# Kernel optimization log

Measured on AMD Instinct MI355X. Metric: run time of the kernel, lower is better.

Reference implementation:

```python
import jax, jax.numpy as jnp
import numpy as np

NV, NE = 4096, 8192
IN_V, OUT_V, IN_E = 128, 128, 64

def setup_inputs() -> dict:
    key = jax.random.key(0)
    ks = jax.random.split(key, 8)
    stdv = 1.0 / np.sqrt(OUT_V)
    return {
        "H_v": jax.random.normal(ks[0], (NV, IN_V), dtype=jnp.float32),
        "H_e": jax.random.normal(ks[1], (NE, IN_E), dtype=jnp.float32),
        "adj_e": jax.random.uniform(ks[2], (NE, NE), dtype=jnp.float32),
        "adj_v": jax.random.uniform(ks[3], (NV, NV), dtype=jnp.float32),
        "T": jax.random.uniform(ks[4], (NV, NE), dtype=jnp.float32),
        "weight": jax.random.uniform(ks[5], (IN_V, OUT_V), minval=-stdv, maxval=stdv, dtype=jnp.float32),
        "bias": jax.random.uniform(ks[6], (OUT_V,), minval=-stdv, maxval=stdv, dtype=jnp.float32),
        "p": jax.random.normal(ks[7], (1, IN_E), dtype=jnp.float32),
    }

def reference(H_v, H_e, adj_e, adj_v, T, weight, bias, p):
    # node_layer=True path of GraphConvolution.forward
    # diag_values = (H_e @ p.T).T[0]  -> [Ne]
    d = H_e @ p[0]                                   # [Ne]
    # T @ diag(d) @ T^T  ==  (T * d) @ T^T  (avoid materializing NxN diag)
    multiplier1 = (T * d[None, :]) @ T.T             # [Nv, Nv]
    # M1 = eye*1 + (1-eye)*multiplier1  -> set diagonal to 1
    idx = jnp.arange(multiplier1.shape[0])
    M1 = multiplier1.at[idx, idx].set(1.0)
    adjusted_A = M1 * adj_v                          # [Nv, Nv]
    output = adjusted_A @ (H_v @ weight) + bias      # [Nv, out_v]
    return (output, H_e)
```

## Files before the change

kernel.cpp:

```cpp
#include <hip/hip_runtime.h>
#include <cstdint>
#include <cstddef>

#define NV 4096
#define NE 8192
#define INV 128
#define OUTV 128
#define INE 64

#define BK 64
#define NT (NE / BK)
#define HALF_B 16384
#define LDS_BYTES (9 * HALF_B)

typedef __bf16 bf16x8 __attribute__((ext_vector_type(8)));
typedef float f32x4 __attribute__((ext_vector_type(4)));

__device__ __forceinline__ uint16_t f2bf(float x) {
  uint32_t u = __builtin_bit_cast(uint32_t, x);
  u += 0x7fff + ((u >> 16) & 1);
  return (uint16_t)(u >> 16);
}

__global__ void k_diag(const float* __restrict__ He, const float* __restrict__ p,
                       float* __restrict__ d) {
  int lane = threadIdx.x & 63;
  int wid = threadIdx.x >> 6;
  int row = blockIdx.x * 4 + wid;
  float v = He[(size_t)row * INE + lane] * p[lane];
#pragma unroll
  for (int off = 32; off; off >>= 1) v += __shfl_xor(v, off);
  if (lane == 0) d[row] = v;
}

__global__ void k_prep(const float4* __restrict__ T4, const float4* __restrict__ d4,
                       ushort4* __restrict__ A4, ushort4* __restrict__ B4) {
  const size_t total = (size_t)NV * NE / 4;
  size_t stride = (size_t)gridDim.x * blockDim.x;
  for (size_t i = (size_t)blockIdx.x * blockDim.x + threadIdx.x; i < total; i += stride) {
    float4 t = T4[i];
    float4 dv = d4[i & (NE / 4 - 1)];
    ushort4 a, b;
    b.x = f2bf(t.x); b.y = f2bf(t.y); b.z = f2bf(t.z); b.w = f2bf(t.w);
    a.x = f2bf(t.x * dv.x); a.y = f2bf(t.y * dv.y);
    a.z = f2bf(t.z * dv.z); a.w = f2bf(t.w * dv.w);
    A4[i] = a;
    B4[i] = b;
  }
}

__global__ void k_xw(const float* __restrict__ Hv, const float* __restrict__ W,
                     uint16_t* __restrict__ XT) {
  __shared__ float row[INV];
  int m = blockIdx.x;
  int n = threadIdx.x;
  row[n] = Hv[(size_t)m * INV + n];
  __syncthreads();
  float acc = 0.f;
#pragma unroll 8
  for (int k = 0; k < INV; ++k) acc += row[k] * W[k * OUTV + n];
  XT[(size_t)n * NV + m] = f2bf(acc);
}


__device__ __forceinline__ void gload16(const char* src, char* ldst) {
  __builtin_amdgcn_global_load_lds(
      (const __attribute__((address_space(1))) uint32_t*)src,
      (__attribute__((address_space(3))) uint32_t*)ldst, 16, 0, 0);
}

__global__ __launch_bounds__(512, 2) void k_gemm1(const uint16_t* __restrict__ A,
                                                  const uint16_t* __restrict__ B,
                                                  const float* __restrict__ adj_v,
                                                  uint16_t* __restrict__ adjA) {
  extern __shared__ char smem[];
  char* Aslot = smem;
  char* Bslot = smem + 5 * HALF_B;

  const int tid = threadIdx.x;
  const int lane = tid & 63, wid = tid >> 6;
  const int wr = wid >> 2, wc = wid & 3;
  const int lr = lane & 15, lk = lane >> 4;
  const int bcol0 = (wc & 1) * 64;

  int bid = blockIdx.x;
  int xcd = bid & 7, cid = bid >> 3;
  int bi = (xcd >> 1) * 4 + (cid >> 3);
  int bj = (xcd & 1) * 8 + (cid & 7);

  const int arow0 = bi * 256, brow0 = bj * 256;

  const int swz0 = ((lk) ^ (lr & 7)) << 4;
  const int swz1 = ((4 + lk) ^ (lr & 7)) << 4;
  const int pA0 = lr * 128 + swz0;
  const int pA1 = lr * 128 + swz1;
  const int pB0 = (bcol0 + lr) * 128 + swz0;
  const int pB1 = (bcol0 + lr) * 128 + swz1;

  const int srow = tid >> 3;
  const int sslot = (tid & 7) ^ (srow & 7);
  const int soff0 = srow * 16384 + sslot * 16;
  const int soff1 = soff0 + 64 * 16384;
  const char* Abase = (const char*)A + (size_t)arow0 * 16384;
  const char* Bbase = (const char*)B + (size_t)brow0 * 16384;
  const int ld0 = tid * 16;
  const int ld1 = tid * 16 + 8192;

  f32x4 acc[8][4] = {};
  bf16x8 af[4][2], af2[4][2], bfr[2][2], bfr2[2][2];

  {
    gload16(Abase + soff0, Aslot + ld0);
    gload16(Abase + soff1, Aslot + ld1);
    gload16(Abase + 2097152 + soff0, Aslot + HALF_B + ld0);
    gload16(Abase + 2097152 + soff1, Aslot + HALF_B + ld1);
    gload16(Bbase + soff0, Bslot + ld0);
    gload16(Bbase + soff1, Bslot + ld1);
    gload16(Bbase + 2097152 + soff0, Bslot + HALF_B + ld0);
    gload16(Bbase + 2097152 + soff1, Bslot + HALF_B + ld1);
    gload16(Abase + 128 + soff0, Aslot + 2 * HALF_B + ld0);
    gload16(Abase + 128 + soff1, Aslot + 2 * HALF_B + ld1);
  }
  asm volatile("s_waitcnt vmcnt(2)" ::: "memory");
  asm volatile("s_barrier" ::: "memory");

  int sA = 0;
  int sB = 0;
  for (int t = 0; t < NT; ++t) {
    const char* aB = Aslot + (((sA + wr) >= 5) ? (sA + wr - 5) : (sA + wr)) * HALF_B;
    const char* bB = Bslot + ((sB + (wc >> 1)) & 3) * HALF_B;
    const char* aK0 = aB + pA0;
    const char* aK1 = aB + pA1;
    const char* bK0 = bB + pB0;
    const char* bK1 = bB + pB1;
    const int k1 = (t + 1) * 128;
    const int k2 = (t + 2) * 128;

#pragma unroll
    for (int m = 0; m < 4; ++m) {
      af[m][0] = *(const bf16x8*)(aK0 + m * 2048);
      af[m][1] = *(const bf16x8*)(aK1 + m * 2048);
    }
#pragma unroll
    for (int n = 0; n < 2; ++n) {
      bfr[n][0] = *(const bf16x8*)(bK0 + n * 2048);
      bfr[n][1] = *(const bf16x8*)(bK1 + n * 2048);
    }
    if (t + 1 < NT) {
      int s1 = sA + 3; if (s1 >= 5) s1 -= 5;
      char* dA1 = Aslot + s1 * HALF_B;
      gload16(Abase + 2097152 + k1 + soff0, dA1 + ld0);
      gload16(Abase + 2097152 + k1 + soff1, dA1 + ld1);
      char* dB0 = Bslot + ((sB + 2) & 3) * HALF_B;
      gload16(Bbase + k1 + soff0, dB0 + ld0);
      gload16(Bbase + k1 + soff1, dB0 + ld1);
      char* dB1 = Bslot + ((sB + 3) & 3) * HALF_B;
      gload16(Bbase + 2097152 + k1 + soff0, dB1 + ld0);
      gload16(Bbase + 2097152 + k1 + soff1, dB1 + ld1);
    }
    __builtin_amdgcn_s_setprio(1);
#pragma unroll
    for (int m = 0; m < 4; ++m)
#pragma unroll
      for (int n = 0; n < 2; ++n)
#pragma unroll
        for (int kk = 0; kk < 2; ++kk)
          acc[m][n] = __builtin_amdgcn_mfma_f32_16x16x32_bf16(af[m][kk], bfr[n][kk], acc[m][n], 0, 0, 0);
    __builtin_amdgcn_s_setprio(0);

#pragma unroll
    for (int n = 0; n < 2; ++n) {
      bfr2[n][0] = *(const bf16x8*)(bK0 + 4096 + n * 2048);
      bfr2[n][1] = *(const bf16x8*)(bK1 + 4096 + n * 2048);
    }
    if (t + 2 < NT) {
      int s2 = sA + 4; if (s2 >= 5) s2 -= 5;
      char* dA0 = Aslot + s2 * HALF_B;
      gload16(Abase + k2 + soff0, dA0 + ld0);
      gload16(Abase + k2 + soff1, dA0 + ld1);
    }
    __builtin_amdgcn_s_setprio(1);
#pragma unroll
    for (int m = 0; m < 4; ++m)
#pragma unroll
      for (int n = 0; n < 2; ++n)
#pragma unroll
        for (int kk = 0; kk < 2; ++kk)
          acc[m][2 + n] = __builtin_amdgcn_mfma_f32_16x16x32_bf16(af[m][kk], bfr2[n][kk], acc[m][2 + n], 0, 0, 0);
    __builtin_amdgcn_s_setprio(0);

#pragma unroll
    for (int m = 0; m < 4; ++m) {
      af2[m][0] = *(const bf16x8*)(aK0 + 8192 + m * 2048);
      af2[m][1] = *(const bf16x8*)(aK1 + 8192 + m * 2048);
    }
    __builtin_amdgcn_s_setprio(1);
#pragma unroll
    for (int m = 0; m < 4; ++m)
#pragma unroll
      for (int n = 0; n < 2; ++n)
#pragma unroll
        for (int kk = 0; kk < 2; ++kk)
          acc[4 + m][2 + n] = __builtin_amdgcn_mfma_f32_16x16x32_bf16(af2[m][kk], bfr2[n][kk], acc[4 + m][2 + n], 0, 0, 0);
    __builtin_amdgcn_s_setprio(0);

    __builtin_amdgcn_s_setprio(1);
#pragma unroll
    for (int m = 0; m < 4; ++m)
#pragma unroll
      for (int n = 0; n < 2; ++n)
#pragma unroll
        for (int kk = 0; kk < 2; ++kk)
          acc[4 + m][n] = __builtin_amdgcn_mfma_f32_16x16x32_bf16(af2[m][kk], bfr[n][kk], acc[4 + m][n], 0, 0, 0);
    __builtin_amdgcn_s_setprio(0);

    if (t + 2 < NT) {
      asm volatile("s_waitcnt vmcnt(2)" ::: "memory");
    } else {
      asm volatile("s_waitcnt vmcnt(0)" ::: "memory");
    }
    asm volatile("s_barrier" ::: "memory");

    sA += 2; if (sA >= 5) sA -= 5;
    sB ^= 2;
  }

#pragma unroll
  for (int m = 0; m < 8; ++m) {
    int grow0 = bi * 256 + wr * 128 + m * 16 + lk * 4;
#pragma unroll
    for (int n = 0; n < 4; ++n) {
      int gcol = bj * 256 + wc * 64 + n * 16 + lr;
#pragma unroll
      for (int r = 0; r < 4; ++r) {
        int grow = grow0 + r;
        float v = acc[m][n][r];
        if (grow == gcol) v = 1.0f;
        adjA[(size_t)grow * NV + gcol] = f2bf(v * adj_v[(size_t)grow * NV + gcol]);
      }
    }
  }
}

__global__ __launch_bounds__(256) void k_gemm2p(const uint16_t* __restrict__ A,
                                                const uint16_t* __restrict__ B,
                                                float* __restrict__ part) {
  __shared__ __align__(16) uint16_t As[128 * 32];
  __shared__ __align__(16) uint16_t Bs[128 * 32];
  const int tid = threadIdx.x;
  const int wid = tid >> 6, lane = tid & 63;
  const int wr = wid >> 1, wc = wid & 1;
  const int ks = blockIdx.x & 7;
  const int bi = blockIdx.x >> 3;
  const int lr = lane & 15, lk = lane >> 4;

  f32x4 acc[4][4] = {};

  for (int kt = ks * 16; kt < ks * 16 + 16; ++kt) {
#pragma unroll
    for (int i = 0; i < 2; ++i) {
      int o = (wid * 2 + i) * 1024 + lane * 16;
      int row = o >> 6, kb = o & 63;
      const char* ga = (const char*)A + ((size_t)(bi * 128 + row) * NV + kt * 32) * 2 + kb;
      const char* gb = (const char*)B + ((size_t)row * NV + kt * 32) * 2 + kb;
      __builtin_amdgcn_global_load_lds(
          (const __attribute__((address_space(1))) uint32_t*)ga,
          (__attribute__((address_space(3))) uint32_t*)((char*)As + (wid * 2 + i) * 1024),
          16, 0, 0);
      __builtin_amdgcn_global_load_lds(
          (const __attribute__((address_space(1))) uint32_t*)gb,
          (__attribute__((address_space(3))) uint32_t*)((char*)Bs + (wid * 2 + i) * 1024),
          16, 0, 0);
    }
    __syncthreads();
    bf16x8 af[4], bfr[4];
#pragma unroll
    for (int m = 0; m < 4; ++m)
      af[m] = *(const bf16x8*)&As[(wr * 64 + m * 16 + lr) * 32 + lk * 8];
#pragma unroll
    for (int n = 0; n < 4; ++n)
      bfr[n] = *(const bf16x8*)&Bs[(wc * 64 + n * 16 + lr) * 32 + lk * 8];
#pragma unroll
    for (int m = 0; m < 4; ++m)
#pragma unroll
      for (int n = 0; n < 4; ++n)
        acc[m][n] = __builtin_amdgcn_mfma_f32_16x16x32_bf16(af[m], bfr[n], acc[m][n], 0, 0, 0);
    __syncthreads();
  }

  float* my = part + (size_t)ks * NV * OUTV;
#pragma unroll
  for (int m = 0; m < 4; ++m) {
    int grow0 = bi * 128 + wr * 64 + m * 16 + lk * 4;
#pragma unroll
    for (int n = 0; n < 4; ++n) {
      int gcol = wc * 64 + n * 16 + lr;
#pragma unroll
      for (int r = 0; r < 4; ++r)
        my[(size_t)(grow0 + r) * OUTV + gcol] = acc[m][n][r];
    }
  }
}

__global__ void k_gemm2r(const float4* __restrict__ part, const float* __restrict__ bias,
                         float4* __restrict__ out) {
  int i = blockIdx.x * 256 + threadIdx.x;
  float4 s = part[i];
#pragma unroll
  for (int ks = 1; ks < 8; ++ks) {
    float4 q = part[(size_t)ks * (NV * OUTV / 4) + i];
    s.x += q.x; s.y += q.y; s.z += q.z; s.w += q.w;
  }
  float4 b = ((const float4*)bias)[i & 31];
  s.x += b.x; s.y += b.y; s.z += b.z; s.w += b.w;
  out[i] = s;
}

extern "C" void kernel_launch(void* const* d_in, const int* in_sizes, int n_in,
                              void* d_out, int out_size, void* d_ws, size_t ws_size,
                              hipStream_t stream) {
  const float* Hv = (const float*)d_in[0];
  const float* He = (const float*)d_in[1];
  const float* adj_v = (const float*)d_in[3];
  const float* T = (const float*)d_in[4];
  const float* W = (const float*)d_in[5];
  const float* bias = (const float*)d_in[6];
  const float* p = (const float*)d_in[7];
  float* out = (float*)d_out;

  char* ws = (char*)d_ws;
  float* dvec = (float*)ws;
  uint16_t* XT = (uint16_t*)(ws + 32768);
  uint16_t* Abf = (uint16_t*)(ws + 32768 + (1u << 20));
  uint16_t* Bbf = Abf + (size_t)NV * NE;
  uint16_t* adjA = Bbf + (size_t)NV * NE;
  float* part = (float*)Abf;

  static int lds_attr_set = 0;
  if (!lds_attr_set) {
    hipFuncSetAttribute((const void*)k_gemm1,
                        hipFuncAttributeMaxDynamicSharedMemorySize, LDS_BYTES);
    lds_attr_set = 1;
  }

  k_diag<<<NE / 4, 256, 0, stream>>>(He, p, dvec);
  k_prep<<<2048, 256, 0, stream>>>((const float4*)T, (const float4*)dvec,
                                   (ushort4*)Abf, (ushort4*)Bbf);
  k_xw<<<NV, INV, 0, stream>>>(Hv, W, XT);
  k_gemm1<<<256, 512, LDS_BYTES, stream>>>(Abf, Bbf, adj_v, adjA);
  k_gemm2p<<<256, 256, 0, stream>>>(adjA, XT, part);
  k_gemm2r<<<NV * OUTV / 4 / 256, 256, 0, stream>>>((const float4*)part, bias, (float4*)out);
  hipMemcpyAsync(out + (size_t)NV * OUTV, He, (size_t)NE * INE * sizeof(float),
                 hipMemcpyDeviceToDevice, stream);
}
```

Before: 297.1 us.

## Load B fragments directly from global memory instead of staging through LDS

The B operand of the main GEMM is no longer copied into LDS slots. Each wave now loads its B MFMA fragments straight from global memory into registers every K step, and LDS drops from nine half-buffers to five. This removes LDS traffic and capacity for B and may allow more occupancy, but B reads are now per-wave global loads that are not shared across waves, and their latency is exposed without prefetching. The MFMA and A-fragment load order is also rearranged.

```diff
diff --git a/kernel.cpp b/kernel.cpp
--- a/kernel.cpp
+++ b/kernel.cpp
@@ -11,7 +11,7 @@
 #define BK 64
 #define NT (NE / BK)
 #define HALF_B 16384
-#define LDS_BYTES (9 * HALF_B)
+#define LDS_BYTES (5 * HALF_B)
 
 typedef __bf16 bf16x8 __attribute__((ext_vector_type(8)));
 typedef float f32x4 __attribute__((ext_vector_type(4)));
@@ -75,7 +75,6 @@
                                                   uint16_t* __restrict__ adjA) {
   extern __shared__ char smem[];
   char* Aslot = smem;
-  char* Bslot = smem + 5 * HALF_B;
 
   const int tid = threadIdx.x;
   const int lane = tid & 63, wid = tid >> 6;
@@ -94,84 +93,61 @@
   const int swz1 = ((4 + lk) ^ (lr & 7)) << 4;
   const int pA0 = lr * 128 + swz0;
   const int pA1 = lr * 128 + swz1;
-  const int pB0 = (bcol0 + lr) * 128 + swz0;
-  const int pB1 = (bcol0 + lr) * 128 + swz1;
 
   const int srow = tid >> 3;
   const int sslot = (tid & 7) ^ (srow & 7);
   const int soff0 = srow * 16384 + sslot * 16;
   const int soff1 = soff0 + 64 * 16384;
   const char* Abase = (const char*)A + (size_t)arow0 * 16384;
-  const char* Bbase = (const char*)B + (size_t)brow0 * 16384;
   const int ld0 = tid * 16;
   const int ld1 = tid * 16 + 8192;
 
+  const uint16_t* Bpan = B + (size_t)brow0 * NE;
+  int bvoff[4];
+#pragma unroll
+  for (int n = 0; n < 4; ++n)
+    bvoff[n] = ((wc >> 1) * 128 + bcol0 + n * 16 + lr) * NE + lk * 8;
+
   f32x4 acc[8][4] = {};
   bf16x8 af[4][2], af2[4][2], bfr[2][2], bfr2[2][2];
 
-  {
-    gload16(Abase + soff0, Aslot + ld0);
-    gload16(Abase + soff1, Aslot + ld1);
-    gload16(Abase + 2097152 + soff0, Aslot + HALF_B + ld0);
-    gload16(Abase + 2097152 + soff1, Aslot + HALF_B + ld1);
-    gload16(Bbase + soff0, Bslot + ld0);
-    gload16(Bbase + soff1, Bslot + ld1);
-    gload16(Bbase + 2097152 + soff0, Bslot + HALF_B + ld0);
-    gload16(Bbase + 2097152 + soff1, Bslot + HALF_B + ld1);
-    gload16(Abase + 128 + soff0, Aslot + 2 * HALF_B + ld0);
-    gload16(Abase + 128 + soff1, Aslot + 2 * HALF_B + ld1);
-  }
+  gload16(Abase + soff0, Aslot + ld0);
+  gload16(Abase + soff1, Aslot + ld1);
+  gload16(Abase + 2097152 + soff0, Aslot + HALF_B + ld0);
+  gload16(Abase + 2097152 + soff1, Aslot + HALF_B + ld1);
+  gload16(Abase + 128 + soff0, Aslot + 2 * HALF_B + ld0);
+  gload16(Abase + 128 + soff1, Aslot + 2 * HALF_B + ld1);
   asm volatile("s_waitcnt vmcnt(2)" ::: "memory");
   asm volatile("s_barrier" ::: "memory");
 
   int sA = 0;
-  int sB = 0;
   for (int t = 0; t < NT; ++t) {
     const char* aB = Aslot + (((sA + wr) >= 5) ? (sA + wr - 5) : (sA + wr)) * HALF_B;
-    const char* bB = Bslot + ((sB + (wc >> 1)) & 3) * HALF_B;
     const char* aK0 = aB + pA0;
     const char* aK1 = aB + pA1;
-    const char* bK0 = bB + pB0;
-    const char* bK1 = bB + pB1;
+    const uint16_t* Bt = Bpan + t * 64;
     const int k1 = (t + 1) * 128;
     const int k2 = (t + 2) * 128;
+
+#pragma unroll
+    for (int n = 0; n < 2; ++n) {
+      bfr[n][0] = *(const bf16x8*)(Bt + bvoff[n]);
+      bfr[n][1] = *(const bf16x8*)(Bt + bvoff[n] + 32);
+      bfr2[n][0] = *(const bf16x8*)(Bt + bvoff[2 + n]);
+      bfr2[n][1] = *(const bf16x8*)(Bt + bvoff[2 + n] + 32);
+    }
 
 #pragma unroll
     for (int m = 0; m < 4; ++m) {
       af[m][0] = *(const bf16x8*)(aK0 + m * 2048);
       af[m][1] = *(const bf16x8*)(aK1 + m * 2048);
     }
-#pragma unroll
-    for (int n = 0; n < 2; ++n) {
-      bfr[n][0] = *(const bf16x8*)(bK0 + n * 2048);
-      bfr[n][1] = *(const bf16x8*)(bK1 + n * 2048);
-    }
+
     if (t + 1 < NT) {
       int s1 = sA + 3; if (s1 >= 5) s1 -= 5;
       char* dA1 = Aslot + s1 * HALF_B;
       gload16(Abase + 2097152 + k1 + soff0, dA1 + ld0);
       gload16(Abase + 2097152 + k1 + soff1, dA1 + ld1);
-      char* dB0 = Bslot + ((sB + 2) & 3) * HALF_B;
-      gload16(Bbase + k1 + soff0, dB0 + ld0);
-      gload16(Bbase + k1 + soff1, dB0 + ld1);
-      char* dB1 = Bslot + ((sB + 3) & 3) * HALF_B;
-      gload16(Bbase + 2097152 + k1 + soff0, dB1 + ld0);
-      gload16(Bbase + 2097152 + k1 + soff1, dB1 + ld1);
-    }
-    __builtin_amdgcn_s_setprio(1);
-#pragma unroll
-    for (int m = 0; m < 4; ++m)
-#pragma unroll
-      for (int n = 0; n < 2; ++n)
-#pragma unroll
-        for (int kk = 0; kk < 2; ++kk)
-          acc[m][n] = __builtin_amdgcn_mfma_f32_16x16x32_bf16(af[m][kk], bfr[n][kk], acc[m][n], 0, 0, 0);
-    __builtin_amdgcn_s_setprio(0);
-
-#pragma unroll
-    for (int n = 0; n < 2; ++n) {
-      bfr2[n][0] = *(const bf16x8*)(bK0 + 4096 + n * 2048);
-      bfr2[n][1] = *(const bf16x8*)(bK1 + 4096 + n * 2048);
     }
     if (t + 2 < NT) {
       int s2 = sA + 4; if (s2 >= 5) s2 -= 5;
@@ -179,6 +155,23 @@
       gload16(Abase + k2 + soff0, dA0 + ld0);
       gload16(Abase + k2 + soff1, dA0 + ld1);
     }
+
+    __builtin_amdgcn_s_setprio(1);
+#pragma unroll
+    for (int m = 0; m < 4; ++m)
+#pragma unroll
+      for (int n = 0; n < 2; ++n)
+#pragma unroll
+        for (int kk = 0; kk < 2; ++kk)
+          acc[m][n] = __builtin_amdgcn_mfma_f32_16x16x32_bf16(af[m][kk], bfr[n][kk], acc[m][n], 0, 0, 0);
+    __builtin_amdgcn_s_setprio(0);
+
+#pragma unroll
+    for (int m = 0; m < 4; ++m) {
+      af2[m][0] = *(const bf16x8*)(aK0 + 8192 + m * 2048);
+      af2[m][1] = *(const bf16x8*)(aK1 + 8192 + m * 2048);
+    }
+
     __builtin_amdgcn_s_setprio(1);
 #pragma unroll
     for (int m = 0; m < 4; ++m)
@@ -189,11 +182,6 @@
           acc[m][2 + n] = __builtin_amdgcn_mfma_f32_16x16x32_bf16(af[m][kk], bfr2[n][kk], acc[m][2 + n], 0, 0, 0);
     __builtin_amdgcn_s_setprio(0);
 
-#pragma unroll
-    for (int m = 0; m < 4; ++m) {
-      af2[m][0] = *(const bf16x8*)(aK0 + 8192 + m * 2048);
-      af2[m][1] = *(const bf16x8*)(aK1 + 8192 + m * 2048);
-    }
     __builtin_amdgcn_s_setprio(1);
 #pragma unroll
     for (int m = 0; m < 4; ++m)
@@ -222,7 +210,6 @@
     asm volatile("s_barrier" ::: "memory");
 
     sA += 2; if (sA >= 5) sA -= 5;
-    sB ^= 2;
   }
 
 #pragma unroll
```

Result: slower. 467.5 us (+57.3%).
